# Kernel optimization log

Hardware: AMD Instinct MI355X
Metric: run time of the kernel (lower is better)

## Reference

```python
import math
import jax, jax.numpy as jnp
import numpy as np

B, T, HID, H, D = 2, 2048, 1024, 16, 64
EPS = 1e-5


def score_norm(s):
    # standardize scores over the key axis (per row), as in RealFormer-style score normalization
    mu = jnp.mean(s, axis=-1, keepdims=True)
    sd = jnp.std(s, axis=-1, keepdims=True)
    return (s - mu) / (sd + EPS)


def setup_inputs() -> dict:
    key = jax.random.key(0)
    ks = jax.random.split(key, 9)
    w_scale = 1.0 / math.sqrt(HID)
    return {
        "x": jax.random.normal(ks[0], (B, T, HID), dtype=jnp.float32),
        "s_prev": jax.random.normal(ks[1], (B, H, T, T), dtype=jnp.float32),
        "Wq": jax.random.normal(ks[2], (HID, H * D), dtype=jnp.float32) * w_scale,
        "Wk": jax.random.normal(ks[3], (HID, H * D), dtype=jnp.float32) * w_scale,
        "Wv": jax.random.normal(ks[4], (HID, H * D), dtype=jnp.float32) * w_scale,
        "Wo": jax.random.normal(ks[5], (H * D, HID), dtype=jnp.float32) * w_scale,
        "alpha": jnp.zeros((H,), dtype=jnp.float32),   # alpha_init = 0.0
        "gamma": jnp.ones((H,), dtype=jnp.float32),    # gamma_init = 1.0
        "beta": jnp.zeros((H,), dtype=jnp.float32),    # beta_init = 0.0
    }


def reference(x, s_prev, Wq, Wk, Wv, Wo, alpha, gamma, beta):
    Bx, t, _ = x.shape
    # project and split heads: [B, H, t, D]
    def split(h):
        return h.reshape(Bx, t, H, D).transpose(0, 2, 1, 3)
    Q = split(x @ Wq)
    K = split(x @ Wk)
    V = split(x @ Wv)

    raw = jnp.einsum('bhtd,bhsd->bhts', Q, K) / math.sqrt(D)

    # gated residual score term (s_prev detached: residual_grad_flow=False)
    gate = jax.nn.sigmoid(alpha)[None, :, None, None]
    scale = gamma[None, :, None, None]
    shift = beta[None, :, None, None]
    r = gate * (scale * score_norm(jax.lax.stop_gradient(s_prev)) + shift)
    raw = raw + r

    # causal mask (t > 1 path)
    causal = jnp.triu(jnp.ones((t, t), dtype=bool), k=1)  # True above diagonal
    scores = jnp.where(causal[None, None], -jnp.inf, raw)

    w = jax.nn.softmax(scores, axis=-1)
    ctx = jnp.einsum('bhts,bhsd->bhtd', w, V)
    merged = ctx.transpose(0, 2, 1, 3).reshape(Bx, t, H * D)
    out = merged @ Wo
    return out, raw
```

## Files before the change

kernel.cpp:

```cpp
#include <hip/hip_runtime.h>

typedef __attribute__((ext_vector_type(4))) float f32x4;
typedef __attribute__((ext_vector_type(8))) short s16x8;
typedef __attribute__((ext_vector_type(4))) unsigned short u16x4;
typedef unsigned short ushortT;

__device__ inline ushortT f2bf(float f) {
  union { float f; unsigned u; } v; v.f = f;
  unsigned r = v.u + 0x7fffu + ((v.u >> 16) & 1u);
  return (ushortT)(r >> 16);
}
__device__ inline float bf2f(ushortT s) {
  union { unsigned u; float f; } v; v.u = ((unsigned)s) << 16;
  return v.f;
}
__device__ inline unsigned pk_bf16(float lo, float hi) {
  unsigned r;
  asm("v_cvt_pk_bf16_f32 %0, %1, %2" : "=v"(r) : "v"(lo), "v"(hi));
  return r;
}
__device__ inline ushortT cvt1_bf16(float f) {
  unsigned r;
  asm("v_cvt_pk_bf16_f32 %0, %1, %2" : "=v"(r) : "v"(f), "v"(f));
  return (ushortT)r;
}
__device__ inline f32x4 mfma16(s16x8 a, s16x8 b, f32x4 c) {
  return __builtin_amdgcn_mfma_f32_16x16x32_bf16(a, b, c, 0, 0, 0);
}
typedef const __attribute__((address_space(1))) unsigned GU;
typedef __attribute__((address_space(3))) unsigned LU;
__device__ inline void gload_lds16(const void* g, void* l) {
  __builtin_amdgcn_global_load_lds((GU*)g, (LU*)l, 16, 0, 0);
}

#define BARRIER_LIGHT() do {                                  \
    __builtin_amdgcn_sched_barrier(0);                        \
    asm volatile("s_waitcnt lgkmcnt(0)" ::: "memory");        \
    __builtin_amdgcn_s_barrier();                             \
    __builtin_amdgcn_sched_barrier(0);                        \
  } while (0)

__global__ void conv_bf16(const float* __restrict__ in, ushortT* __restrict__ o) {
  size_t i = ((size_t)blockIdx.x * 256 + threadIdx.x) * 4;
  f32x4 v = *(const f32x4*)(in + i);
  u16x4 u = { f2bf(v[0]), f2bf(v[1]), f2bf(v[2]), f2bf(v[3]) };
  *(u16x4*)(o + i) = u;
}

__global__ void transp_bf16(const float* __restrict__ Wm, ushortT* __restrict__ wt) {
  __shared__ float t[32][33];
  int bx = blockIdx.x, by = blockIdx.y;
  int x = threadIdx.x, y = threadIdx.y;
#pragma unroll
  for (int i = 0; i < 32; i += 8)
    t[y + i][x] = Wm[(size_t)(by * 32 + y + i) * 1024 + bx * 32 + x];
  __syncthreads();
#pragma unroll
  for (int i = 0; i < 32; i += 8)
    wt[(size_t)(bx * 32 + y + i) * 1024 + by * 32 + x] = f2bf(t[x][y + i]);
}

template <int MODE>
__global__ __launch_bounds__(256) void gemm_bt(const ushortT* __restrict__ A,
                                               const ushortT* __restrict__ Bt,
                                               ushortT* __restrict__ o0,
                                               ushortT* __restrict__ o1,
                                               ushortT* __restrict__ o2,
                                               float* __restrict__ of) {
  __shared__ ushortT lA[128 * 32];
  __shared__ ushortT lB[128 * 32];
  const int tid = threadIdx.x;
  const int w = tid >> 6, l = tid & 63;
  const int a = l & 15, hi = l >> 4;
  const int wr = w >> 1, wc = w & 1;
  const int row0 = blockIdx.y * 128, col0 = blockIdx.x * 128;
  f32x4 acc[4][4] = {};
  const int r1 = tid >> 2, c1 = tid & 3;
  const int r2 = (tid + 256) >> 2, c2 = (tid + 256) & 3;
  for (int k0 = 0; k0 < 1024; k0 += 32) {
    __syncthreads();
    gload_lds16(A + (size_t)(row0 + r1) * 1024 + k0 + c1 * 8, &lA[r1 * 32 + c1 * 8]);
    gload_lds16(A + (size_t)(row0 + r2) * 1024 + k0 + c2 * 8, &lA[r2 * 32 + c2 * 8]);
    gload_lds16(Bt + (size_t)(col0 + r1) * 1024 + k0 + c1 * 8, &lB[r1 * 32 + c1 * 8]);
    gload_lds16(Bt + (size_t)(col0 + r2) * 1024 + k0 + c2 * 8, &lB[r2 * 32 + c2 * 8]);
    __syncthreads();
    s16x8 af[4], bfr[4];
#pragma unroll
    for (int m = 0; m < 4; ++m)
      af[m] = *(const s16x8*)&lA[(wr * 64 + m * 16 + a) * 32 + hi * 8];
#pragma unroll
    for (int n = 0; n < 4; ++n)
      bfr[n] = *(const s16x8*)&lB[(wc * 64 + n * 16 + a) * 32 + hi * 8];
#pragma unroll
    for (int m = 0; m < 4; ++m)
#pragma unroll
      for (int n = 0; n < 4; ++n)
        acc[m][n] = mfma16(af[m], bfr[n], acc[m][n]);
  }
  const int proj = col0 >> 10;
#pragma unroll
  for (int m = 0; m < 4; ++m)
#pragma unroll
    for (int n = 0; n < 4; ++n) {
      const int gr0 = row0 + wr * 64 + m * 16 + hi * 4;
      const int gc = col0 + wc * 64 + n * 16 + a;
#pragma unroll
      for (int r = 0; r < 4; ++r) {
        const int gr = gr0 + r;
        float v = acc[m][n][r];
        if (MODE == 0) {
          const int bb = gr >> 11, t = gr & 2047;
          const int cc = gc & 1023;
          const int hh = cc >> 6, d = cc & 63;
          const size_t bh = (size_t)bb * 16 + hh;
          if (proj == 0)      o0[(bh * 2048 + t) * 64 + d] = f2bf(v * 0.125f);
          else if (proj == 1) o1[(bh * 2048 + t) * 64 + d] = f2bf(v);
          else                o2[(bh * 64 + d) * 2048 + t] = f2bf(v);
        } else {
          of[(size_t)gr * 1024 + gc] = v;
        }
      }
    }
}

#define SBS 2056
__global__ __launch_bounds__(1024, 4) void attn_fused(
    const ushortT* __restrict__ qw, const ushortT* __restrict__ kw,
    const ushortT* __restrict__ vtw, const float* __restrict__ sprev,
    const float* __restrict__ alpha, const float* __restrict__ gamma,
    const float* __restrict__ beta, float* __restrict__ raw,
    ushortT* __restrict__ merged) {
  __shared__ ushortT sb[2][16 * SBS];
  __shared__ float c0_s[2][16], c1_s[2][16], li_s[16];
  __shared__ float red[2][4][64][4];

  const int bid = blockIdx.x;
  const int xcd = bid & 7, idx = bid >> 3;
  const int bh = xcd * 4 + (idx & 3);
  const int jslot = idx >> 2;
  const int h = bh & 15, b = bh >> 4;
  const int tid = threadIdx.x;
  const int w = tid >> 6, l = tid & 63;
  const int a = l & 15, hi = l >> 4;

  const float gate = 1.f / (1.f + __expf(-alpha[h]));
  const float gm = gamma[h], bt = beta[h];
  const ushortT* kbp = kw + (size_t)bh * 2048 * 64;
  const float* spb = sprev + (size_t)bh * 2048 * 2048;

  auto prod_row = [&](int t0n, int row, int nb) {
    const float* rp = spb + (size_t)(t0n + row) * 2048 + 4 * l;
    ushortT* dst = &sb[nb][row * SBS + 4 * l];
    float sum = 0.f, sq = 0.f;
#pragma unroll
    for (int i = 0; i < 8; ++i) {
      f32x4 v = __builtin_nontemporal_load((const f32x4*)(rp + 256 * i));
      sum += v[0] + v[1] + v[2] + v[3];
      sq += v[0] * v[0] + v[1] * v[1] + v[2] * v[2] + v[3] * v[3];
      uint2 u;
      u.x = pk_bf16(v[0], v[1]);
      u.y = pk_bf16(v[2], v[3]);
      *(uint2*)&dst[256 * i] = u;
    }
#pragma unroll
    for (int s = 32; s >= 1; s >>= 1) {
      sum += __shfl_xor(sum, s);
      sq += __shfl_xor(sq, s);
    }
    if (l == 0) {
      float mu = sum * (1.f / 2048.f);
      float var = fmaxf(sq * (1.f / 2048.f) - mu * mu, 0.f);
      float rs = 1.f / (sqrtf(var) + 1e-5f);
      c1_s[nb][row] = gate * gm * rs;
      c0_s[nb][row] = gate * (bt - gm * mu * rs);
    }
  };

  if (w < 4) {
    const int t00 = jslot * 16;
    prod_row(t00, w, 0);
    prod_row(t00, w + 4, 0);
    prod_row(t00, w + 8, 0);
    prod_row(t00, w + 12, 0);
  }
  BARRIER_LIGHT();

  for (int it = 0; it < 16; ++it) {
    const int t0 = jslot * 16 + it * 128;
    const int cb = it & 1, nb = cb ^ 1;
    const int t0n = jslot * 16 + (it + 1) * 128;
    const bool dopre = (it < 15);
    ushortT* sbc = sb[cb];

    if (w < 4) {
      if (dopre) { prod_row(t0n, w, nb); prod_row(t0n, w + 4, nb); }
      BARRIER_LIGHT();
      if (dopre) prod_row(t0n, w + 8, nb);
      BARRIER_LIGHT();
      if (dopre) prod_row(t0n, w + 12, nb);
      BARRIER_LIGHT();
      BARRIER_LIGHT();
    } else {
      const int cw = w - 4;
      {
        const ushortT* qrow = qw + ((size_t)bh * 2048 + t0 + a) * 64;
        s16x8 qf0 = *(const s16x8*)(qrow + hi * 8);
        s16x8 qf1 = *(const s16x8*)(qrow + 32 + hi * 8);
        float c04[4], c14[4];
#pragma unroll
        for (int r = 0; r < 4; ++r) {
          c04[r] = c0_s[cb][4 * hi + r];
          c14[r] = c1_s[cb][4 * hi + r];
        }
        float* rawb = raw + ((size_t)bh * 2048 + t0) * 2048;
        for (int tIdx = cw; tIdx < 128; tIdx += 12) {
          const int col0 = tIdx * 16;
          const ushortT* kr = kbp + (size_t)(col0 + a) * 64 + hi * 8;
          s16x8 kf0 = *(const s16x8*)(kr);
          s16x8 kf1 = *(const s16x8*)(kr + 32);
          f32x4 s4 = {};
          s4 = mfma16(qf0, kf0, s4);
          s4 = mfma16(qf1, kf1, s4);
#pragma unroll
          for (int r = 0; r < 4; ++r) {
            const int rl = 4 * hi + r;
            const float spv = bf2f(sbc[rl * SBS + col0 + a]);
            const float rv = fmaf(c14[r], spv, s4[r] + c04[r]);
            rawb[(size_t)rl * 2048 + col0 + a] = rv;
            sbc[rl * SBS + col0 + a] = cvt1_bf16((col0 + a) <= (t0 + rl) ? rv : -1e30f);
          }
        }
      }
      BARRIER_LIGHT();
      for (int row = cw; row < 16; row += 12) {
        float m = -3e38f;
#pragma unroll
        for (int i = 0; i < 16; ++i) {
          unsigned u = *(const unsigned*)&sbc[row * SBS + 2 * l + 128 * i];
          union { unsigned u; float f; } lo, hh;
          lo.u = u << 16; hh.u = u & 0xffff0000u;
          m = fmaxf(m, fmaxf(lo.f, hh.f));
        }
#pragma unroll
        for (int s = 32; s >= 1; s >>= 1) m = fmaxf(m, __shfl_xor(m, s));
        float sum = 0.f;
#pragma unroll
        for (int i = 0; i < 16; ++i) {
          unsigned u = *(const unsigned*)&sbc[row * SBS + 2 * l + 128 * i];
          union { unsigned u; float f; } lo, hh;
          lo.u = u << 16; hh.u = u & 0xffff0000u;
          float e0 = __expf(lo.f - m);
          float e1 = __expf(hh.f - m);
          sum += e0 + e1;
          *(unsigned*)&sbc[row * SBS + 2 * l + 128 * i] = pk_bf16(e0, e1);
        }
#pragma unroll
        for (int s = 32; s >= 1; s >>= 1) sum += __shfl_xor(sum, s);
        if (l == 0) li_s[row] = 1.f / sum;
      }
      BARRIER_LIGHT();
      const int n = cw & 3, third = cw >> 2;
      const ushortT* vb = vtw + ((size_t)bh * 64 + 16 * n + a) * 2048;
      f32x4 acc = {};
      const int nch = (t0 + 47) >> 5;
      for (int c = third; c < nch; c += 3) {
        s16x8 pf = *(const s16x8*)&sbc[a * SBS + 32 * c + 8 * hi];
        s16x8 vf = *(const s16x8*)(vb + 32 * c + 8 * hi);
        acc = mfma16(pf, vf, acc);
      }
      if (third) *(f32x4*)red[third - 1][n][l] = acc;
      BARRIER_LIGHT();
      if (third == 0) {
        f32x4 p1 = *(f32x4*)red[0][n][l];
        f32x4 p2 = *(f32x4*)red[1][n][l];
        acc += p1 + p2;
#pragma unroll
        for (int r = 0; r < 4; ++r) {
          const int rl = 4 * hi + r;
          merged[((size_t)b * 2048 + t0 + rl) * 1024 + h * 64 + 16 * n + a] =
              f2bf(acc[r] * li_s[rl]);
        }
      }
      BARRIER_LIGHT();
    }
  }
}

extern "C" void kernel_launch(void* const* d_in, const int* in_sizes, int n_in,
                              void* d_out, int out_size, void* d_ws, size_t ws_size,
                              hipStream_t stream) {
  (void)in_sizes; (void)n_in; (void)out_size; (void)ws_size;
  const float* x      = (const float*)d_in[0];
  const float* s_prev = (const float*)d_in[1];
  const float* Wq     = (const float*)d_in[2];
  const float* Wk     = (const float*)d_in[3];
  const float* Wv     = (const float*)d_in[4];
  const float* Wo     = (const float*)d_in[5];
  const float* alpha  = (const float*)d_in[6];
  const float* gamma  = (const float*)d_in[7];
  const float* beta   = (const float*)d_in[8];

  float* out = (float*)d_out;
  float* raw = out + (size_t)4194304;

  char* ws = (char*)d_ws;
  const size_t MB = 1024 * 1024;
  ushortT* xb  = (ushortT*)(ws);
  ushortT* wT  = (ushortT*)(ws + 8 * MB);
  ushortT* woT = (ushortT*)(ws + 14 * MB);
  ushortT* qw  = (ushortT*)(ws + 16 * MB);
  ushortT* kw  = (ushortT*)(ws + 24 * MB);
  ushortT* vtw = (ushortT*)(ws + 32 * MB);
  ushortT* mg  = (ushortT*)(ws + 40 * MB);

  conv_bf16<<<4096, 256, 0, stream>>>(x, xb);
  dim3 tb(32, 8);
  transp_bf16<<<dim3(32, 32), tb, 0, stream>>>(Wq, wT);
  transp_bf16<<<dim3(32, 32), tb, 0, stream>>>(Wk, wT + 1024 * 1024);
  transp_bf16<<<dim3(32, 32), tb, 0, stream>>>(Wv, wT + 2 * 1024 * 1024);
  transp_bf16<<<dim3(32, 32), tb, 0, stream>>>(Wo, woT);

  gemm_bt<0><<<dim3(24, 32), 256, 0, stream>>>(xb, wT, qw, kw, vtw, nullptr);

  attn_fused<<<256, 1024, 0, stream>>>(qw, kw, vtw, s_prev, alpha, gamma,
                                       beta, raw, mg);

  gemm_bt<1><<<dim3(8, 32), 256, 0, stream>>>(mg, woT, nullptr, nullptr, nullptr, out);
}
```

Before: 444.8 us.

## Transpose score MFMA for vector stores; prefetch K/V fragments; widen softmax LDS access

Swaps the MFMA operand order in the score stage so each lane owns one query row and four consecutive key columns. This allows 16-byte stores of raw scores and 8-byte LDS read-modify-writes of the s_prev/probability buffer instead of scalar ones. K fragments are prefetched one tile ahead, and the PV loop keeps four V fragments in flight in registers. The softmax pass uses wider LDS loads, and the prologue spreads the first tile's s_prev row normalization across all warps. These reduce instruction count and memory latency stalls, at the cost of more registers and more complex loop control.

```diff
diff --git a/kernel.cpp b/kernel.cpp
--- a/kernel.cpp
+++ b/kernel.cpp
@@ -14,15 +14,18 @@
   union { unsigned u; float f; } v; v.u = ((unsigned)s) << 16;
   return v.f;
 }
+__device__ inline float bflo(unsigned u) {
+  union { unsigned u; float f; } v; v.u = u << 16;
+  return v.f;
+}
+__device__ inline float bfhi(unsigned u) {
+  union { unsigned u; float f; } v; v.u = u & 0xffff0000u;
+  return v.f;
+}
 __device__ inline unsigned pk_bf16(float lo, float hi) {
   unsigned r;
   asm("v_cvt_pk_bf16_f32 %0, %1, %2" : "=v"(r) : "v"(lo), "v"(hi));
   return r;
-}
-__device__ inline ushortT cvt1_bf16(float f) {
-  unsigned r;
-  asm("v_cvt_pk_bf16_f32 %0, %1, %2" : "=v"(r) : "v"(f), "v"(f));
-  return (ushortT)r;
 }
 __device__ inline f32x4 mfma16(s16x8 a, s16x8 b, f32x4 c) {
   return __builtin_amdgcn_mfma_f32_16x16x32_bf16(a, b, c, 0, 0, 0);
@@ -176,13 +179,7 @@
     }
   };
 
-  if (w < 4) {
-    const int t00 = jslot * 16;
-    prod_row(t00, w, 0);
-    prod_row(t00, w + 4, 0);
-    prod_row(t00, w + 8, 0);
-    prod_row(t00, w + 12, 0);
-  }
+  prod_row(jslot * 16, w, 0);
   BARRIER_LIGHT();
 
   for (int it = 0; it < 16; ++it) {
@@ -206,53 +203,72 @@
         const ushortT* qrow = qw + ((size_t)bh * 2048 + t0 + a) * 64;
         s16x8 qf0 = *(const s16x8*)(qrow + hi * 8);
         s16x8 qf1 = *(const s16x8*)(qrow + 32 + hi * 8);
-        float c04[4], c14[4];
-#pragma unroll
-        for (int r = 0; r < 4; ++r) {
-          c04[r] = c0_s[cb][4 * hi + r];
-          c14[r] = c1_s[cb][4 * hi + r];
-        }
-        float* rawb = raw + ((size_t)bh * 2048 + t0) * 2048;
-        for (int tIdx = cw; tIdx < 128; tIdx += 12) {
-          const int col0 = tIdx * 16;
-          const ushortT* kr = kbp + (size_t)(col0 + a) * 64 + hi * 8;
-          s16x8 kf0 = *(const s16x8*)(kr);
-          s16x8 kf1 = *(const s16x8*)(kr + 32);
+        const float c0v = c0_s[cb][a];
+        const float c1v = c1_s[cb][a];
+        const int lim = t0 + a;
+        float* rawb = raw + ((size_t)bh * 2048 + t0 + a) * 2048;
+        int tIdx = cw;
+        const ushortT* kr = kbp + (size_t)(tIdx * 16 + a) * 64 + hi * 8;
+        s16x8 kf0 = *(const s16x8*)(kr);
+        s16x8 kf1 = *(const s16x8*)(kr + 32);
+        for (; tIdx < 128; tIdx += 12) {
+          s16x8 nf0, nf1;
+          const bool more = (tIdx + 12 < 128);
+          if (more) {
+            const ushortT* krn = kbp + (size_t)((tIdx + 12) * 16 + a) * 64 + hi * 8;
+            nf0 = *(const s16x8*)(krn);
+            nf1 = *(const s16x8*)(krn + 32);
+          }
           f32x4 s4 = {};
-          s4 = mfma16(qf0, kf0, s4);
-          s4 = mfma16(qf1, kf1, s4);
-#pragma unroll
-          for (int r = 0; r < 4; ++r) {
-            const int rl = 4 * hi + r;
-            const float spv = bf2f(sbc[rl * SBS + col0 + a]);
-            const float rv = fmaf(c14[r], spv, s4[r] + c04[r]);
-            rawb[(size_t)rl * 2048 + col0 + a] = rv;
-            sbc[rl * SBS + col0 + a] = cvt1_bf16((col0 + a) <= (t0 + rl) ? rv : -1e30f);
-          }
+          s4 = mfma16(kf0, qf0, s4);
+          s4 = mfma16(kf1, qf1, s4);
+          const int col0 = tIdx * 16 + 4 * hi;
+          uint2 sp = *(const uint2*)&sbc[a * SBS + col0];
+          f32x4 rv;
+          rv[0] = fmaf(c1v, bflo(sp.x), s4[0] + c0v);
+          rv[1] = fmaf(c1v, bfhi(sp.x), s4[1] + c0v);
+          rv[2] = fmaf(c1v, bflo(sp.y), s4[2] + c0v);
+          rv[3] = fmaf(c1v, bfhi(sp.y), s4[3] + c0v);
+          *(f32x4*)&rawb[col0] = rv;
+          const float m0 = (col0 + 0) <= lim ? rv[0] : -1e30f;
+          const float m1 = (col0 + 1) <= lim ? rv[1] : -1e30f;
+          const float m2 = (col0 + 2) <= lim ? rv[2] : -1e30f;
+          const float m3 = (col0 + 3) <= lim ? rv[3] : -1e30f;
+          uint2 w2;
+          w2.x = pk_bf16(m0, m1);
+          w2.y = pk_bf16(m2, m3);
+          *(uint2*)&sbc[a * SBS + col0] = w2;
+          if (more) { kf0 = nf0; kf1 = nf1; }
         }
       }
       BARRIER_LIGHT();
       for (int row = cw; row < 16; row += 12) {
+        ushortT* rp = &sbc[row * SBS + 8 * l];
         float m = -3e38f;
 #pragma unroll
-        for (int i = 0; i < 16; ++i) {
-          unsigned u = *(const unsigned*)&sbc[row * SBS + 2 * l + 128 * i];
-          union { unsigned u; float f; } lo, hh;
-          lo.u = u << 16; hh.u = u & 0xffff0000u;
-          m = fmaxf(m, fmaxf(lo.f, hh.f));
+        for (int i = 0; i < 4; ++i) {
+          uint2 u0 = *(const uint2*)&rp[512 * i];
+          uint2 u1 = *(const uint2*)&rp[512 * i + 4];
+          m = fmaxf(m, fmaxf(fmaxf(bflo(u0.x), bfhi(u0.x)), fmaxf(bflo(u0.y), bfhi(u0.y))));
+          m = fmaxf(m, fmaxf(fmaxf(bflo(u1.x), bfhi(u1.x)), fmaxf(bflo(u1.y), bfhi(u1.y))));
         }
 #pragma unroll
         for (int s = 32; s >= 1; s >>= 1) m = fmaxf(m, __shfl_xor(m, s));
         float sum = 0.f;
 #pragma unroll
-        for (int i = 0; i < 16; ++i) {
-          unsigned u = *(const unsigned*)&sbc[row * SBS + 2 * l + 128 * i];
-          union { unsigned u; float f; } lo, hh;
-          lo.u = u << 16; hh.u = u & 0xffff0000u;
-          float e0 = __expf(lo.f - m);
-          float e1 = __expf(hh.f - m);
-          sum += e0 + e1;
-          *(unsigned*)&sbc[row * SBS + 2 * l + 128 * i] = pk_bf16(e0, e1);
+        for (int i = 0; i < 4; ++i) {
+          uint2 u0 = *(const uint2*)&rp[512 * i];
+          uint2 u1 = *(const uint2*)&rp[512 * i + 4];
+          float e0 = __expf(bflo(u0.x) - m), e1 = __expf(bfhi(u0.x) - m);
+          float e2 = __expf(bflo(u0.y) - m), e3 = __expf(bfhi(u0.y) - m);
+          float e4 = __expf(bflo(u1.x) - m), e5 = __expf(bfhi(u1.x) - m);
+          float e6 = __expf(bflo(u1.y) - m), e7 = __expf(bfhi(u1.y) - m);
+          sum += (e0 + e1 + e2 + e3) + (e4 + e5 + e6 + e7);
+          uint2 w0, w1;
+          w0.x = pk_bf16(e0, e1); w0.y = pk_bf16(e2, e3);
+          w1.x = pk_bf16(e4, e5); w1.y = pk_bf16(e6, e7);
+          *(uint2*)&rp[512 * i] = w0;
+          *(uint2*)&rp[512 * i + 4] = w1;
         }
 #pragma unroll
         for (int s = 32; s >= 1; s >>= 1) sum += __shfl_xor(sum, s);
@@ -263,10 +279,35 @@
       const ushortT* vb = vtw + ((size_t)bh * 64 + 16 * n + a) * 2048;
       f32x4 acc = {};
       const int nch = (t0 + 47) >> 5;
-      for (int c = third; c < nch; c += 3) {
-        s16x8 pf = *(const s16x8*)&sbc[a * SBS + 32 * c + 8 * hi];
-        s16x8 vf = *(const s16x8*)(vb + 32 * c + 8 * hi);
-        acc = mfma16(pf, vf, acc);
+      {
+        s16x8 v0, v1, v2, v3;
+        const int c0i = third;
+        if (c0i + 0 < nch) v0 = *(const s16x8*)(vb + 32 * (c0i + 0) + 8 * hi);
+        if (c0i + 3 < nch) v1 = *(const s16x8*)(vb + 32 * (c0i + 3) + 8 * hi);
+        if (c0i + 6 < nch) v2 = *(const s16x8*)(vb + 32 * (c0i + 6) + 8 * hi);
+        if (c0i + 9 < nch) v3 = *(const s16x8*)(vb + 32 * (c0i + 9) + 8 * hi);
+        for (int cc = c0i; cc < nch; cc += 12) {
+          if (cc + 0 < nch) {
+            s16x8 pf = *(const s16x8*)&sbc[a * SBS + 32 * (cc + 0) + 8 * hi];
+            acc = mfma16(pf, v0, acc);
+            if (cc + 12 < nch) v0 = *(const s16x8*)(vb + 32 * (cc + 12) + 8 * hi);
+          }
+          if (cc + 3 < nch) {
+            s16x8 pf = *(const s16x8*)&sbc[a * SBS + 32 * (cc + 3) + 8 * hi];
+            acc = mfma16(pf, v1, acc);
+            if (cc + 15 < nch) v1 = *(const s16x8*)(vb + 32 * (cc + 15) + 8 * hi);
+          }
+          if (cc + 6 < nch) {
+            s16x8 pf = *(const s16x8*)&sbc[a * SBS + 32 * (cc + 6) + 8 * hi];
+            acc = mfma16(pf, v2, acc);
+            if (cc + 18 < nch) v2 = *(const s16x8*)(vb + 32 * (cc + 18) + 8 * hi);
+          }
+          if (cc + 9 < nch) {
+            s16x8 pf = *(const s16x8*)&sbc[a * SBS + 32 * (cc + 9) + 8 * hi];
+            acc = mfma16(pf, v3, acc);
+            if (cc + 21 < nch) v3 = *(const s16x8*)(vb + 32 * (cc + 21) + 8 * hi);
+          }
+        }
       }
       if (third) *(f32x4*)red[third - 1][n][l] = acc;
       BARRIER_LIGHT();
```

After: 535.9 us. 1.2x slower.
